# Kernel tuning notes

Hardware: AMD Instinct MI355X
Metric: run time of the kernel (lower is better)

The kernel has to match this reference:

```python
import jax, jax.numpy as jnp
import numpy as np

B, W, KD, NC, D, NN, NH, AD, HOPS = 512, 4, 64, 32, 256, 16, 8, 32, 4
DH = D // NH
DFF = 4 * D
P = B * W + B
ROLE_WRITER, ROLE_QUERY = 0, 1


def setup_inputs() -> dict:
    key = jax.random.key(0)
    ks = iter(jax.random.split(key, 40))
    f = lambda shape, s=0.02: jax.random.normal(next(ks), shape, dtype=jnp.float32) * s
    inp = {
        'query_keys': jax.random.normal(next(ks), (B, KD), dtype=jnp.float32),
        'writer_keys': jax.random.normal(next(ks), (B, W, KD), dtype=jnp.float32),
        'key_proj_w': f((KD, D)), 'key_proj_b': jnp.zeros((D,), jnp.float32),
        'class_embed': f((NC, D)), 'role_embed': f((3, D)), 'start_node_embed': f((NN, D)),
        'input_ln_g': jnp.ones((D,), jnp.float32), 'input_ln_b': jnp.zeros((D,), jnp.float32),
        'ln1_g': jnp.ones((NN, D), jnp.float32), 'ln1_b': jnp.zeros((NN, D), jnp.float32),
        'wqkv': f((NN, D, 3 * D)), 'bqkv': jnp.zeros((NN, 3 * D), jnp.float32),
        'wo': f((NN, D, D)), 'bo': jnp.zeros((NN, D), jnp.float32),
        'ln2_g': jnp.ones((NN, D), jnp.float32), 'ln2_b': jnp.zeros((NN, D), jnp.float32),
        'w_fc1': f((NN, D, DFF)), 'b_fc1': jnp.zeros((NN, DFF), jnp.float32),
        'w_fc2': f((NN, DFF, D)), 'b_fc2': jnp.zeros((NN, D), jnp.float32),
        'delta_w': jnp.zeros((D, D), jnp.float32), 'delta_b': jnp.zeros((D,), jnp.float32),
        'dir_w': f((D, D)), 'dir_b': jnp.zeros((D,), jnp.float32),
        'mag_w': f((D, 1)), 'mag_b': jnp.full((1,), 2.5, jnp.float32),
        'out_w': f((D, NC)), 'out_b': jnp.zeros((NC,), jnp.float32),
        'address_table': jax.random.normal(next(ks), (NN, AD), dtype=jnp.float32),
        'query_start_nodes': jax.random.randint(next(ks), (B,), 0, NN),
        'writer_labels': jax.random.randint(next(ks), (B, W), 0, NC),
        'writer_start_nodes': jax.random.randint(next(ks), (B, W), 0, NN),
    }
    return inp


def _ln(x):
    m = jnp.mean(x, -1, keepdims=True)
    v = jnp.var(x, -1, keepdims=True)
    return (x - m) * jax.lax.rsqrt(v + 1e-5)


def _forward(query_keys, writer_keys, key_proj_w, key_proj_b, class_embed, role_embed,
             start_node_embed, input_ln_g, input_ln_b, ln1_g, ln1_b, wqkv, bqkv, wo, bo,
             ln2_g, ln2_b, w_fc1, b_fc1, w_fc2, b_fc2, delta_w, delta_b, dir_w, dir_b,
             mag_w, mag_b, out_w, out_b, address_table,
             query_start_nodes, writer_labels, writer_start_nodes):
    # ---- encode writers (encode_writers) ----
    fk = writer_keys.reshape(-1, KD)          # [B*W, KD]
    fl = writer_labels.reshape(-1)            # [B*W]
    fs = writer_start_nodes.reshape(-1)       # [B*W]
    learned_w = fk @ key_proj_w + key_proj_b + class_embed[fl] + start_node_embed[fs] + role_embed[ROLE_WRITER]
    sw = jnp.zeros_like(learned_w).at[:, :KD].set(fk)
    sw = sw.at[:, KD:KD + NC].set(jax.nn.one_hot(fl, NC, dtype=learned_w.dtype))
    enc_w = _ln(learned_w) * input_ln_g + input_ln_b + sw
    # ---- encode queries (encode_queries) ----
    learned_q = query_keys @ key_proj_w + key_proj_b + start_node_embed[query_start_nodes] + role_embed[ROLE_QUERY]
    sq = jnp.zeros_like(learned_q).at[:, :KD].set(query_keys)
    enc_q = _ln(learned_q) * input_ln_g + input_ln_b + sq

    h = jnp.concatenate([enc_w, enc_q], axis=0)          # [P, D]
    node = jnp.concatenate([fs, query_start_nodes], 0)   # [P] current compute node per packet

    inv_sqrt_dh = 1.0 / np.sqrt(DH).astype(np.float32)
    for _ in range(HOPS):
        oh = jax.nn.one_hot(node, NN, dtype=h.dtype)      # [P, NN] dispatch weights

        def pnl(x, Wn, bn):
            # per-node linear: gather-compute-scatter via MoE-style dense dispatch
            xe = jnp.einsum('pn,pd->npd', oh, x)          # [NN, P, din]
            ye = jnp.einsum('npd,ndf->npf', xe, Wn)       # [NN, P, dout]
            return jnp.einsum('npf,pn->pf', ye, oh) + oh @ bn

        # ComputeNodeCell: pre-LN attention among packets at the same node
        x = _ln(h) * (oh @ ln1_g) + oh @ ln1_b
        qkv = pnl(x, wqkv, bqkv)                          # [P, 3D]
        q, k, v = jnp.split(qkv, 3, axis=-1)
        q = q.reshape(P, NH, DH); k = k.reshape(P, NH, DH); v = v.reshape(P, NH, DH)
        scores = jnp.einsum('phd,qhd->hpq', q, k) * inv_sqrt_dh   # [NH, P, P]
        same = node[:, None] == node[None, :]
        scores = jnp.where(same[None], scores, -1e9)
        attn = jax.nn.softmax(scores, axis=-1)
        ao = jnp.einsum('hpq,qhd->phd', attn, v).reshape(P, D)
        h = h + pnl(ao, wo, bo)
        # MLP block
        x2 = _ln(h) * (oh @ ln2_g) + oh @ ln2_b
        h = h + pnl(jax.nn.gelu(pnl(x2, w_fc1, b_fc1)), w_fc2, b_fc2)
        # routing heads: pick next node from address table, apply gated delta
        direction = h @ dir_w + dir_b
        node = jnp.argmax(direction[:, :AD] @ address_table.T, axis=-1)
        h = h + (h @ delta_w + delta_b) * jax.nn.sigmoid(h @ mag_w + mag_b)

    return h @ out_w + out_b                              # [P, NC] per-packet logits


def reference(query_keys, writer_keys, key_proj_w, key_proj_b, class_embed, role_embed,
              start_node_embed, input_ln_g, input_ln_b, ln1_g, ln1_b, wqkv, bqkv, wo, bo,
              ln2_g, ln2_b, w_fc1, b_fc1, w_fc2, b_fc2, delta_w, delta_b, dir_w, dir_b,
              mag_w, mag_b, out_w, out_b, address_table,
              query_start_nodes, writer_labels, writer_start_nodes):
    return _forward(query_keys, writer_keys, key_proj_w, key_proj_b, class_embed, role_embed,
                    start_node_embed, input_ln_g, input_ln_b, ln1_g, ln1_b, wqkv, bqkv, wo, bo,
                    ln2_g, ln2_b, w_fc1, b_fc1, w_fc2, b_fc2, delta_w, delta_b, dir_w, dir_b,
                    mag_w, mag_b, out_w, out_b, address_table,
                    query_start_nodes, writer_labels, writer_start_nodes)
```

## Files before the change

### kernel.cpp

```cpp
#include <hip/hip_runtime.h>
#include <math.h>

#define B_    512
#define W_    4
#define KD_   64
#define NC_   32
#define D_    256
#define NN_   16
#define NH_   8
#define AD_   32
#define HOPS_ 4
#define DH_   32
#define DFF_  1024
#define P_    2560
#define BW_   2048
#define MAXT2_ 176

#define INV_SQRT_DH 0.17677669529663687f

__device__ __forceinline__ float block_sum256(float v, float* red) {
#pragma unroll
  for (int off = 32; off > 0; off >>= 1) v += __shfl_xor(v, off, 64);
  int wid = threadIdx.x >> 6;
  if ((threadIdx.x & 63) == 0) red[wid] = v;
  __syncthreads();
  float s = red[0] + red[1] + red[2] + red[3];
  __syncthreads();
  return s;
}

__device__ __forceinline__ float gelu_tanh(float v) {
  float u = 0.7978845608028654f * (v + 0.044715f * v * v * v);
  return 0.5f * v * (1.0f + tanhf(u));
}

__global__ __launch_bounds__(256) void encode_kernel(
    const float* __restrict__ query_keys, const float* __restrict__ writer_keys,
    const float* __restrict__ kpw, const float* __restrict__ kpb,
    const float* __restrict__ ce, const float* __restrict__ re,
    const float* __restrict__ sne, const float* __restrict__ ilg,
    const float* __restrict__ ilb, const int* __restrict__ qsn,
    const int* __restrict__ wl, const int* __restrict__ wsn,
    float* __restrict__ h, int* __restrict__ node) {
  int p = blockIdx.x, t = threadIdx.x;
  __shared__ float fk[KD_];
  __shared__ float red[4];
  const float* key;
  int lab = -1, sn, role;
  if (p < BW_) { key = writer_keys + (size_t)p * KD_; lab = wl[p]; sn = wsn[p]; role = 0; }
  else { int b = p - BW_; key = query_keys + (size_t)b * KD_; sn = qsn[b]; role = 1; }
  if (t < KD_) fk[t] = key[t];
  __syncthreads();

  float acc = kpb[t] + sne[sn * D_ + t] + re[role * D_ + t];
  if (lab >= 0) acc += ce[lab * D_ + t];
#pragma unroll 8
  for (int i = 0; i < KD_; i++) acc += fk[i] * kpw[i * D_ + t];

  float mean = block_sum256(acc, red) * (1.0f / D_);
  float d = acc - mean;
  float var = block_sum256(d * d, red) * (1.0f / D_);
  float xn = d * (1.0f / sqrtf(var + 1e-5f));

  float sw = 0.0f;
  if (t < KD_) sw = fk[t];
  else if (lab >= 0 && t < KD_ + NC_) sw = (t - KD_ == lab) ? 1.0f : 0.0f;

  h[(size_t)p * D_ + t] = xn * ilg[t] + ilb[t] + sw;
  if (t == 0) node[p] = sn;
}

__global__ __launch_bounds__(256) void sort_kernel(const int* __restrict__ node,
                                                   int* __restrict__ order,
                                                   int* __restrict__ invord,
                                                   int* __restrict__ offs,
                                                   int* __restrict__ cnts,
                                                   int* __restrict__ tnode,
                                                   int* __restrict__ tstart,
                                                   int* __restrict__ tend,
                                                   int* __restrict__ ntiles) {
  __shared__ int c[NN_], o[NN_], cur[NN_];
  int t = threadIdx.x;
  if (t < NN_) c[t] = 0;
  __syncthreads();
  for (int p = t; p < P_; p += 256) atomicAdd(&c[node[p]], 1);
  __syncthreads();
  if (t == 0) {
    int s = 0;
    for (int n = 0; n < NN_; n++) { o[n] = s; cur[n] = s; s += c[n]; }
    int idx = 0;
    for (int n = 0; n < NN_; n++) {
      int e = o[n] + c[n];
      for (int m0 = o[n]; m0 < e; m0 += 16) {
        tnode[idx] = n; tstart[idx] = m0; tend[idx] = e; idx++;
      }
    }
    ntiles[0] = idx;
  }
  __syncthreads();
  if (t < NN_) { cnts[t] = c[t]; offs[t] = o[t]; }
  for (int p = t; p < P_; p += 256) {
    int r = atomicAdd(&cur[node[p]], 1);
    order[r] = p;
    invord[p] = r;
  }
}

__global__ __launch_bounds__(256) void ln_affine(const float* __restrict__ h,
                                                 const float* __restrict__ g,
                                                 const float* __restrict__ b,
                                                 const int* __restrict__ node,
                                                 const int* __restrict__ order,
                                                 float* __restrict__ x) {
  int sp = blockIdx.x * 4 + (threadIdx.x >> 6);
  int lane = threadIdx.x & 63;
  int p = order[sp];
  int n = node[p];
  float4 v = *(const float4*)&h[(size_t)p * D_ + lane * 4];
  float s = v.x + v.y + v.z + v.w;
#pragma unroll
  for (int off = 32; off > 0; off >>= 1) s += __shfl_xor(s, off, 64);
  float mean = s * (1.0f / D_);
  float4 d = make_float4(v.x - mean, v.y - mean, v.z - mean, v.w - mean);
  float vr = d.x * d.x + d.y * d.y + d.z * d.z + d.w * d.w;
#pragma unroll
  for (int off = 32; off > 0; off >>= 1) vr += __shfl_xor(vr, off, 64);
  float inv = 1.0f / sqrtf(vr * (1.0f / D_) + 1e-5f);
  float4 gg = *(const float4*)&g[n * D_ + lane * 4];
  float4 bb = *(const float4*)&b[n * D_ + lane * 4];
  float4 o;
  o.x = d.x * inv * gg.x + bb.x;
  o.y = d.y * inv * gg.y + bb.y;
  o.z = d.z * inv * gg.z + bb.z;
  o.w = d.w * inv * gg.w + bb.w;
  *(float4*)&x[(size_t)sp * D_ + lane * 4] = o;
}

template <int DIN, int DOUT, int ACT, int RESID, int PER_NODE, int KSPLIT, int XMODE>
__global__ __launch_bounds__(256) void glin2(const float* __restrict__ x,
                                             const float* __restrict__ W,
                                             const float* __restrict__ bias,
                                             float* __restrict__ out,
                                             float* __restrict__ pbuf,
                                             const float* __restrict__ xaux,
                                             const int* __restrict__ order,
                                             const int* __restrict__ invord,
                                             const int* __restrict__ tnode,
                                             const int* __restrict__ tstart,
                                             const int* __restrict__ tend,
                                             const int* __restrict__ ntiles) {
  constexpr int KLEN = DIN / KSPLIT;

  int gx = gridDim.x;
  int bid = blockIdx.x;
  int ti = (bid & 7) * (gx >> 3) + (bid >> 3);

  int n, s0, rows;
  if (PER_NODE) {
    if (ti >= ntiles[0]) return;
    n = tnode[ti];
    s0 = tstart[ti];
    int e = tend[ti];
    rows = e - s0;
    if (rows > 16) rows = 16;
  } else {
    n = 0;
    s0 = ti * 16;
    rows = 16;
  }
  int jb = blockIdx.y * 256;
  int kz = (KSPLIT > 1) ? blockIdx.z : 0;
  int k0 = kz * KLEN;

  int tid = threadIdx.x;
  int wv = __builtin_amdgcn_readfirstlane((int)(tid >> 6));
  int j4 = (tid & 63) << 2;

  const float* Wp = W + (size_t)n * DIN * DOUT + (size_t)k0 * DOUT + jb + j4;

  const float* xr0;
  const float* xr1;
  const float* xr2;
  const float* xr3;
  const float* ar0 = nullptr;
  const float* ar1 = nullptr;
  const float* ar2 = nullptr;
  const float* ar3 = nullptr;
  {
    int rbase = s0 + (wv << 2);
    xr0 = x + (size_t)(rbase + 0) * DIN + k0;
    xr1 = x + (size_t)(rbase + 1) * DIN + k0;
    xr2 = x + (size_t)(rbase + 2) * DIN + k0;
    xr3 = x + (size_t)(rbase + 3) * DIN + k0;
    if (XMODE == 1) {
      ar0 = xaux + (size_t)invord[rbase + 0] * DIN + k0;
      ar1 = xaux + (size_t)invord[rbase + 1] * DIN + k0;
      ar2 = xaux + (size_t)invord[rbase + 2] * DIN + k0;
      ar3 = xaux + (size_t)invord[rbase + 3] * DIN + k0;
    }
  }

  float4 a0 = make_float4(0.f, 0.f, 0.f, 0.f);
  float4 a1 = a0, a2 = a0, a3 = a0;
  float4 wc0, wc1, wc2, wc3, xc0, xc1, xc2, xc3;

#define LDW_(kk, w0, w1, w2, w3)                              \
  w0 = *(const float4*)(Wp + (size_t)((kk) + 0) * DOUT);      \
  w1 = *(const float4*)(Wp + (size_t)((kk) + 1) * DOUT);      \
  w2 = *(const float4*)(Wp + (size_t)((kk) + 2) * DOUT);      \
  w3 = *(const float4*)(Wp + (size_t)((kk) + 3) * DOUT);

#define LDX1_(kk, ptr, aptr, dst)                             \
  dst = *(const float4*)((ptr) + (kk));                       \
  if (XMODE == 1) {                                           \
    float4 _a = *(const float4*)((aptr) + (kk));              \
    dst.x += _a.x; dst.y += _a.y; dst.z += _a.z; dst.w += _a.w; \
  }

#define LDX_(kk, x0, x1, x2, x3)   \
  LDX1_(kk, xr0, ar0, x0)          \
  LDX1_(kk, xr1, ar1, x1)          \
  LDX1_(kk, xr2, ar2, x2)          \
  LDX1_(kk, xr3, ar3, x3)

  LDW_(0, wc0, wc1, wc2, wc3);
  LDX_(0, xc0, xc1, xc2, xc3);

#pragma unroll 2
  for (int kk = 0; kk < KLEN; kk += 4) {
    float4 wn0, wn1, wn2, wn3, xn0, xn1, xn2, xn3;
    bool more = (kk + 4 < KLEN);
    if (more) {
      LDW_(kk + 4, wn0, wn1, wn2, wn3);
      LDX_(kk + 4, xn0, xn1, xn2, xn3);
    }
#pragma unroll
    for (int t = 0; t < 4; ++t) {
      float4 wt = (t == 0) ? wc0 : (t == 1) ? wc1 : (t == 2) ? wc2 : wc3;
      float f0 = (t == 0) ? xc0.x : (t == 1) ? xc0.y : (t == 2) ? xc0.z : xc0.w;
      float f1 = (t == 0) ? xc1.x : (t == 1) ? xc1.y : (t == 2) ? xc1.z : xc1.w;
      float f2 = (t == 0) ? xc2.x : (t == 1) ? xc2.y : (t == 2) ? xc2.z : xc2.w;
      float f3 = (t == 0) ? xc3.x : (t == 1) ? xc3.y : (t == 2) ? xc3.z : xc3.w;
      a0.x += f0 * wt.x; a0.y += f0 * wt.y; a0.z += f0 * wt.z; a0.w += f0 * wt.w;
      a1.x += f1 * wt.x; a1.y += f1 * wt.y; a1.z += f1 * wt.z; a1.w += f1 * wt.w;
      a2.x += f2 * wt.x; a2.y += f2 * wt.y; a2.z += f2 * wt.z; a2.w += f2 * wt.w;
      a3.x += f3 * wt.x; a3.y += f3 * wt.y; a3.z += f3 * wt.z; a3.w += f3 * wt.w;
    }
    if (more) {
      wc0 = wn0; wc1 = wn1; wc2 = wn2; wc3 = wn3;
      xc0 = xn0; xc1 = xn1; xc2 = xn2; xc3 = xn3;
    }
  }
#undef LDW_
#undef LDX1_
#undef LDX_

  int jcol = jb + j4;
  bool main_part = (KSPLIT == 1) || (kz == 0);
  float4 bv = make_float4(0.f, 0.f, 0.f, 0.f);
  if (main_part) bv = *(const float4*)(bias + (size_t)n * DOUT + jcol);

#pragma unroll
  for (int r = 0; r < 4; ++r) {
    int lr = (wv << 2) + r;
    if (PER_NODE && lr >= rows) continue;
    float4 av = (r == 0) ? a0 : (r == 1) ? a1 : (r == 2) ? a2 : a3;
    if (main_part) {
      float4 v = make_float4(av.x + bv.x, av.y + bv.y, av.z + bv.z, av.w + bv.w);
      if (ACT == 1) {
        v.x = gelu_tanh(v.x); v.y = gelu_tanh(v.y);
        v.z = gelu_tanh(v.z); v.w = gelu_tanh(v.w);
      }
      if (RESID) {
        int pp = PER_NODE ? order[s0 + lr] : (s0 + lr);
        float* op = out + (size_t)pp * DOUT + jcol;
        float4 old = *(const float4*)op;
        *(float4*)op = make_float4(v.x + old.x, v.y + old.y, v.z + old.z, v.w + old.w);
      } else {
        *(float4*)(out + (size_t)(s0 + lr) * DOUT + jcol) = v;
      }
    } else {
      *(float4*)(pbuf + (size_t)(s0 + lr) * DOUT + jcol) = av;
    }
  }
}

#define ATS 36
__global__ __launch_bounds__(256) void attn_kernel(const float* __restrict__ qkv,
                                                   const int* __restrict__ node,
                                                   const int* __restrict__ order,
                                                   const int* __restrict__ offs,
                                                   const int* __restrict__ cnts,
                                                   float* __restrict__ ao) {
  __shared__ float qs[32 * ATS];
  __shared__ float kts[32 * ATS];
  __shared__ float vs[32 * ATS];
  __shared__ float ps[32 * ATS];
  __shared__ int glo[32], ghi[32];

  int t = threadIdx.x;
  int r = t >> 3;
  int j4 = (t & 7) * 4;
  int r0 = blockIdx.x * 32;
  int hd = blockIdx.y;

  if (t < 32) {
    int n = node[order[r0 + t]];
    glo[t] = offs[n];
    ghi[t] = offs[n] + cnts[n];
  }
  __syncthreads();

  {
    const float* qp = &qkv[(size_t)(r0 + r) * 768 + hd * 32 + j4];
    float4 q4 = *(const float4*)qp;
    q4.x *= INV_SQRT_DH; q4.y *= INV_SQRT_DH; q4.z *= INV_SQRT_DH; q4.w *= INV_SQRT_DH;
    *(float4*)&qs[r * ATS + j4] = q4;
  }

  int lo = glo[0];
  int hi = ghi[31];
  int myglo = glo[r], myghi = ghi[r];

  float4 o4 = {0.f, 0.f, 0.f, 0.f};
  float mrow = -1e30f, lrow = 0.f;

  for (int kt = lo; kt < hi; kt += 32) {
    int sj = kt + r;
    float4 k4 = {0.f, 0.f, 0.f, 0.f}, v4 = {0.f, 0.f, 0.f, 0.f};
    if (sj < hi) {
      const float* kp = &qkv[(size_t)sj * 768 + 256 + hd * 32 + j4];
      k4 = *(const float4*)kp;
      v4 = *(const float4*)(kp + 256);
    }
    __syncthreads();
    kts[(j4 + 0) * ATS + r] = k4.x;
    kts[(j4 + 1) * ATS + r] = k4.y;
    kts[(j4 + 2) * ATS + r] = k4.z;
    kts[(j4 + 3) * ATS + r] = k4.w;
    *(float4*)&vs[r * ATS + j4] = v4;
    __syncthreads();

    float s0 = 0.f, s1 = 0.f, s2 = 0.f, s3 = 0.f;
#pragma unroll 8
    for (int d = 0; d < 32; d++) {
      float qv = qs[r * ATS + d];
      float4 kv = *(const float4*)&kts[d * ATS + j4];
      s0 += qv * kv.x; s1 += qv * kv.y; s2 += qv * kv.z; s3 += qv * kv.w;
    }
    int c0 = kt + j4;
    if (c0 + 0 < myglo || c0 + 0 >= myghi) s0 = -1e30f;
    if (c0 + 1 < myglo || c0 + 1 >= myghi) s1 = -1e30f;
    if (c0 + 2 < myglo || c0 + 2 >= myghi) s2 = -1e30f;
    if (c0 + 3 < myglo || c0 + 3 >= myghi) s3 = -1e30f;

    float mx = fmaxf(fmaxf(s0, s1), fmaxf(s2, s3));
#pragma unroll
    for (int off = 4; off > 0; off >>= 1) mx = fmaxf(mx, __shfl_xor(mx, off, 8));
    float mnew = fmaxf(mrow, mx);
    float alpha = __expf(mrow - mnew);
    float p0 = __expf(s0 - mnew), p1 = __expf(s1 - mnew);
    float p2 = __expf(s2 - mnew), p3 = __expf(s3 - mnew);
    float ls = p0 + p1 + p2 + p3;
#pragma unroll
    for (int off = 4; off > 0; off >>= 1) ls += __shfl_xor(ls, off, 8);
    lrow = lrow * alpha + ls;
    mrow = mnew;
    o4.x *= alpha; o4.y *= alpha; o4.z *= alpha; o4.w *= alpha;

    *(float4*)&ps[r * ATS + j4] = make_float4(p0, p1, p2, p3);
#pragma unroll 8
    for (int j = 0; j < 32; j++) {
      float pj = ps[r * ATS + j];
      float4 vv = *(const float4*)&vs[j * ATS + j4];
      o4.x += pj * vv.x; o4.y += pj * vv.y; o4.z += pj * vv.z; o4.w += pj * vv.w;
    }
  }

  float inv = 1.f / lrow;
  o4.x *= inv; o4.y *= inv; o4.z *= inv; o4.w *= inv;
  *(float4*)&ao[(size_t)(r0 + r) * D_ + hd * 32 + j4] = o4;
}

__global__ __launch_bounds__(256) void route_kernel(float* __restrict__ h,
                                                    const float* __restrict__ pbuf,
                                                    const int* __restrict__ invord,
                                                    const float* __restrict__ dir_w,
                                                    const float* __restrict__ dir_b,
                                                    const float* __restrict__ at,
                                                    const float* __restrict__ mag_w,
                                                    const float* __restrict__ mag_b,
                                                    const float* __restrict__ delta,
                                                    int* __restrict__ node) {
  int p = blockIdx.x, t = threadIdx.x;
  __shared__ float hs[D_];
  __shared__ float dpart[8][AD_];
  __shared__ float dirs[AD_];
  __shared__ float scs[NN_];
  __shared__ float red[4];
  float hv = h[(size_t)p * D_ + t] + pbuf[(size_t)invord[p] * D_ + t];
  hs[t] = hv;
  __syncthreads();

  int j = t & 31, seg = t >> 5;
  float part = 0.0f;
#pragma unroll 8
  for (int i = 0; i < 32; i++) {
    int ii = seg * 32 + i;
    part += hs[ii] * dir_w[ii * D_ + j];
  }
  dpart[seg][j] = part;
  __syncthreads();
  if (t < AD_) {
    float s = dir_b[t];
#pragma unroll
    for (int g = 0; g < 8; g++) s += dpart[g][t];
    dirs[t] = s;
  }
  __syncthreads();
  if (t < NN_) {
    float s = 0.0f;
#pragma unroll
    for (int a = 0; a < AD_; a++) s += dirs[a] * at[t * AD_ + a];
    scs[t] = s;
  }
  __syncthreads();
  if (t == 0) {
    float best = scs[0];
    int arg = 0;
    for (int nn = 1; nn < NN_; nn++)
      if (scs[nn] > best) { best = scs[nn]; arg = nn; }
    node[p] = arg;
  }
  float mag = block_sum256(hv * mag_w[t], red) + mag_b[0];
  float sig = 1.0f / (1.0f + __expf(-mag));
  h[(size_t)p * D_ + t] = hv + delta[(size_t)p * D_ + t] * sig;
}

__global__ __launch_bounds__(256) void out_kernel(const float* __restrict__ h,
                                                  const float* __restrict__ ow,
                                                  const float* __restrict__ ob,
                                                  float* __restrict__ out) {
  int p = blockIdx.x, t = threadIdx.x;
  __shared__ float hs[D_];
  __shared__ float part[8][NC_];
  hs[t] = h[(size_t)p * D_ + t];
  __syncthreads();
  int j = t & 31, seg = t >> 5;
  float s = 0.0f;
#pragma unroll 8
  for (int i = 0; i < 32; i++) {
    int ii = seg * 32 + i;
    s += hs[ii] * ow[ii * NC_ + j];
  }
  part[seg][j] = s;
  __syncthreads();
  if (t < NC_) {
    float r = ob[t];
#pragma unroll
    for (int g = 0; g < 8; g++) r += part[g][t];
    out[(size_t)p * NC_ + t] = r;
  }
}

extern "C" void kernel_launch(void* const* d_in, const int* in_sizes, int n_in,
                              void* d_out, int out_size, void* d_ws, size_t ws_size,
                              hipStream_t stream) {
  (void)in_sizes; (void)n_in; (void)out_size; (void)ws_size;
  const float* query_keys       = (const float*)d_in[0];
  const float* writer_keys      = (const float*)d_in[1];
  const float* key_proj_w       = (const float*)d_in[2];
  const float* key_proj_b       = (const float*)d_in[3];
  const float* class_embed      = (const float*)d_in[4];
  const float* role_embed       = (const float*)d_in[5];
  const float* start_node_embed = (const float*)d_in[6];
  const float* input_ln_g       = (const float*)d_in[7];
  const float* input_ln_b       = (const float*)d_in[8];
  const float* ln1_g            = (const float*)d_in[9];
  const float* ln1_b            = (const float*)d_in[10];
  const float* wqkv             = (const float*)d_in[11];
  const float* bqkv             = (const float*)d_in[12];
  const float* wo               = (const float*)d_in[13];
  const float* bo               = (const float*)d_in[14];
  const float* ln2_g            = (const float*)d_in[15];
  const float* ln2_b            = (const float*)d_in[16];
  const float* w_fc1            = (const float*)d_in[17];
  const float* b_fc1            = (const float*)d_in[18];
  const float* w_fc2            = (const float*)d_in[19];
  const float* b_fc2            = (const float*)d_in[20];
  const float* delta_w          = (const float*)d_in[21];
  const float* delta_b          = (const float*)d_in[22];
  const float* dir_w            = (const float*)d_in[23];
  const float* dir_b            = (const float*)d_in[24];
  const float* mag_w            = (const float*)d_in[25];
  const float* mag_b            = (const float*)d_in[26];
  const float* out_w            = (const float*)d_in[27];
  const float* out_b            = (const float*)d_in[28];
  const float* address_table    = (const float*)d_in[29];
  const int* query_start_nodes  = (const int*)d_in[30];
  const int* writer_labels      = (const int*)d_in[31];
  const int* writer_start_nodes = (const int*)d_in[32];

  uintptr_t basep = (uintptr_t)d_ws;
  auto carve = [&](size_t bytes) {
    basep = (basep + 255) & ~(uintptr_t)255;
    void* r = (void*)basep;
    basep += bytes;
    return r;
  };
  float* h    = (float*)carve((size_t)(P_ + 16) * D_ * 4);
  float* x    = (float*)carve((size_t)(P_ + 16) * D_ * 4);
  float* buf1 = (float*)carve((size_t)(P_ + 16) * DFF_ * 4);
  float* ff   = (float*)carve((size_t)(P_ + 16) * DFF_ * 4);
  float* pbuf = (float*)carve((size_t)(P_ + 16) * D_ * 4);
  int* node   = (int*)carve(P_ * 4);
  int* order  = (int*)carve(P_ * 4);
  int* invord = (int*)carve(P_ * 4);
  int* offs   = (int*)carve(NN_ * 4);
  int* cnts   = (int*)carve(NN_ * 4);
  int* tnode  = (int*)carve(MAXT2_ * 4);
  int* tstart = (int*)carve(MAXT2_ * 4);
  int* tend   = (int*)carve(MAXT2_ * 4);
  int* ntiles = (int*)carve(4);

  encode_kernel<<<P_, 256, 0, stream>>>(query_keys, writer_keys, key_proj_w, key_proj_b,
                                        class_embed, role_embed, start_node_embed,
                                        input_ln_g, input_ln_b, query_start_nodes,
                                        writer_labels, writer_start_nodes, h, node);

  for (int hop = 0; hop < HOPS_; ++hop) {
    sort_kernel<<<1, 256, 0, stream>>>(node, order, invord, offs, cnts,
                                       tnode, tstart, tend, ntiles);
    ln_affine<<<P_ / 4, 256, 0, stream>>>(h, ln1_g, ln1_b, node, order, x);
    glin2<256, 768, 0, 0, 1, 1, 0><<<dim3(MAXT2_, 3), 256, 0, stream>>>(
        x, wqkv, bqkv, buf1, nullptr, nullptr, order, invord, tnode, tstart, tend,
        ntiles);
    attn_kernel<<<dim3(P_ / 32, NH_), 256, 0, stream>>>(buf1, node, order, offs,
                                                        cnts, x );
    glin2<256, 256, 0, 1, 1, 1, 0><<<dim3(MAXT2_, 1), 256, 0, stream>>>(
        x, wo, bo, h, nullptr, nullptr, order, invord, tnode, tstart, tend, ntiles);
    ln_affine<<<P_ / 4, 256, 0, stream>>>(h, ln2_g, ln2_b, node, order, x);
    glin2<256, 1024, 1, 0, 1, 1, 0><<<dim3(MAXT2_, 4), 256, 0, stream>>>(
        x, w_fc1, b_fc1, ff, nullptr, nullptr, order, invord, tnode, tstart, tend,
        ntiles);
    glin2<1024, 256, 0, 1, 1, 2, 0><<<dim3(MAXT2_, 1, 2), 256, 0, stream>>>(
        ff, w_fc2, b_fc2, h, pbuf, nullptr, order, invord, tnode, tstart, tend,
        ntiles);
    glin2<256, 256, 0, 0, 0, 1, 1><<<dim3(P_ / 16, 1), 256, 0, stream>>>(
        h, delta_w, delta_b, buf1 , nullptr, pbuf, order, invord,
        tnode, tstart, tend, ntiles);
    route_kernel<<<P_, 256, 0, stream>>>(h, pbuf, invord, dir_w, dir_b, address_table,
                                         mag_w, mag_b, buf1, node);
  }

  out_kernel<<<P_, 256, 0, stream>>>(h, out_w, out_b, (float*)d_out);
}
```

Baseline: 1.079 ms.

## Stage weight tiles in LDS via async global_load_lds with double buffering

Replaces the register-streamed GEMM kernel with one that stages 16-row weight chunks into double-buffered shared memory using direct global-to-LDS loads. Each block now has two waves sharing one weight tile, where before four waves each read weights straight from global memory. The row tile per block is also made configurable, using 8 rows for the smaller projections so they launch more blocks. This should cut redundant global weight traffic and overlap loading with compute, at the cost of a block barrier per chunk and fewer waves per block.

```diff
diff --git a/kernel.cpp b/kernel.cpp
--- a/kernel.cpp
+++ b/kernel.cpp
@@ -136,8 +136,9 @@
   *(float4*)&x[(size_t)sp * D_ + lane * 4] = o;
 }
 
-template <int DIN, int DOUT, int ACT, int RESID, int PER_NODE, int KSPLIT, int XMODE>
-__global__ __launch_bounds__(256) void glin2(const float* __restrict__ x,
+template <int DIN, int DOUT, int RT, int ACT, int RESID, int PER_NODE, int KSPLIT,
+          int XMODE>
+__global__ __launch_bounds__(128) void glin3(const float* __restrict__ x,
                                              const float* __restrict__ W,
                                              const float* __restrict__ bias,
                                              float* __restrict__ out,
@@ -149,7 +150,12 @@
                                              const int* __restrict__ tstart,
                                              const int* __restrict__ tend,
                                              const int* __restrict__ ntiles) {
+  constexpr int KC = 16;
   constexpr int KLEN = DIN / KSPLIT;
+  constexpr int NCH = KLEN / KC;
+  constexpr int RPW = RT / 2;
+
+  __shared__ float ws[2][KC][256];
 
   int gx = gridDim.x;
   int bid = blockIdx.x;
@@ -157,16 +163,18 @@
 
   int n, s0, rows;
   if (PER_NODE) {
-    if (ti >= ntiles[0]) return;
-    n = tnode[ti];
-    s0 = tstart[ti];
-    int e = tend[ti];
+    int tt = (RT == 16) ? ti : (ti >> 1);
+    if (tt >= ntiles[0]) return;
+    n = tnode[tt];
+    s0 = tstart[tt] + ((RT == 8) ? (ti & 1) * 8 : 0);
+    int e = tend[tt];
     rows = e - s0;
-    if (rows > 16) rows = 16;
+    if (rows > RT) rows = RT;
+    if (rows < 0) rows = 0;
   } else {
     n = 0;
-    s0 = ti * 16;
-    rows = 16;
+    s0 = ti * RT;
+    rows = RT;
   }
   int jb = blockIdx.y * 256;
   int kz = (KSPLIT > 1) ? blockIdx.z : 0;
@@ -174,97 +182,91 @@
 
   int tid = threadIdx.x;
   int wv = __builtin_amdgcn_readfirstlane((int)(tid >> 6));
-  int j4 = (tid & 63) << 2;
-
-  const float* Wp = W + (size_t)n * DIN * DOUT + (size_t)k0 * DOUT + jb + j4;
-
-  const float* xr0;
-  const float* xr1;
-  const float* xr2;
-  const float* xr3;
-  const float* ar0 = nullptr;
-  const float* ar1 = nullptr;
-  const float* ar2 = nullptr;
-  const float* ar3 = nullptr;
-  {
-    int rbase = s0 + (wv << 2);
-    xr0 = x + (size_t)(rbase + 0) * DIN + k0;
-    xr1 = x + (size_t)(rbase + 1) * DIN + k0;
-    xr2 = x + (size_t)(rbase + 2) * DIN + k0;
-    xr3 = x + (size_t)(rbase + 3) * DIN + k0;
-    if (XMODE == 1) {
-      ar0 = xaux + (size_t)invord[rbase + 0] * DIN + k0;
-      ar1 = xaux + (size_t)invord[rbase + 1] * DIN + k0;
-      ar2 = xaux + (size_t)invord[rbase + 2] * DIN + k0;
-      ar3 = xaux + (size_t)invord[rbase + 3] * DIN + k0;
-    }
-  }
-
-  float4 a0 = make_float4(0.f, 0.f, 0.f, 0.f);
-  float4 a1 = a0, a2 = a0, a3 = a0;
-  float4 wc0, wc1, wc2, wc3, xc0, xc1, xc2, xc3;
-
-#define LDW_(kk, w0, w1, w2, w3)                              \
-  w0 = *(const float4*)(Wp + (size_t)((kk) + 0) * DOUT);      \
-  w1 = *(const float4*)(Wp + (size_t)((kk) + 1) * DOUT);      \
-  w2 = *(const float4*)(Wp + (size_t)((kk) + 2) * DOUT);      \
-  w3 = *(const float4*)(Wp + (size_t)((kk) + 3) * DOUT);
-
-#define LDX1_(kk, ptr, aptr, dst)                             \
-  dst = *(const float4*)((ptr) + (kk));                       \
-  if (XMODE == 1) {                                           \
-    float4 _a = *(const float4*)((aptr) + (kk));              \
-    dst.x += _a.x; dst.y += _a.y; dst.z += _a.z; dst.w += _a.w; \
-  }
-
-#define LDX_(kk, x0, x1, x2, x3)   \
-  LDX1_(kk, xr0, ar0, x0)          \
-  LDX1_(kk, xr1, ar1, x1)          \
-  LDX1_(kk, xr2, ar2, x2)          \
-  LDX1_(kk, xr3, ar3, x3)
-
-  LDW_(0, wc0, wc1, wc2, wc3);
-  LDX_(0, xc0, xc1, xc2, xc3);
-
-#pragma unroll 2
-  for (int kk = 0; kk < KLEN; kk += 4) {
-    float4 wn0, wn1, wn2, wn3, xn0, xn1, xn2, xn3;
-    bool more = (kk + 4 < KLEN);
-    if (more) {
-      LDW_(kk + 4, wn0, wn1, wn2, wn3);
-      LDX_(kk + 4, xn0, xn1, xn2, xn3);
-    }
-#pragma unroll
-    for (int t = 0; t < 4; ++t) {
-      float4 wt = (t == 0) ? wc0 : (t == 1) ? wc1 : (t == 2) ? wc2 : wc3;
-      float f0 = (t == 0) ? xc0.x : (t == 1) ? xc0.y : (t == 2) ? xc0.z : xc0.w;
-      float f1 = (t == 0) ? xc1.x : (t == 1) ? xc1.y : (t == 2) ? xc1.z : xc1.w;
-      float f2 = (t == 0) ? xc2.x : (t == 1) ? xc2.y : (t == 2) ? xc2.z : xc2.w;
-      float f3 = (t == 0) ? xc3.x : (t == 1) ? xc3.y : (t == 2) ? xc3.z : xc3.w;
-      a0.x += f0 * wt.x; a0.y += f0 * wt.y; a0.z += f0 * wt.z; a0.w += f0 * wt.w;
-      a1.x += f1 * wt.x; a1.y += f1 * wt.y; a1.z += f1 * wt.z; a1.w += f1 * wt.w;
-      a2.x += f2 * wt.x; a2.y += f2 * wt.y; a2.z += f2 * wt.z; a2.w += f2 * wt.w;
-      a3.x += f3 * wt.x; a3.y += f3 * wt.y; a3.z += f3 * wt.z; a3.w += f3 * wt.w;
-    }
-    if (more) {
-      wc0 = wn0; wc1 = wn1; wc2 = wn2; wc3 = wn3;
-      xc0 = xn0; xc1 = xn1; xc2 = xn2; xc3 = xn3;
-    }
-  }
-#undef LDW_
-#undef LDX1_
-#undef LDX_
-
-  int jcol = jb + j4;
+  int lane = tid & 63;
+  int jc = lane << 2;
+
+  const float* Wn = W + (size_t)n * DIN * DOUT + jb;
+
+  auto wstage = [&](int buf, int kc) {
+#pragma unroll
+    for (int i = 0; i < KC / 2; i++) {
+      int kr = wv * (KC / 2) + i;
+      const float* g = Wn + (size_t)(k0 + kc + kr) * DOUT + jc;
+      __builtin_amdgcn_global_load_lds(
+          (const __attribute__((address_space(1))) unsigned int*)g,
+          (__attribute__((address_space(3))) unsigned int*)&ws[buf][kr][0],
+          16, 0, 0);
+    }
+  };
+
+  int rbase = s0 + wv * RPW;
+  const float* xb = x + (size_t)rbase * DIN + k0;
+  const float* ax[RPW];
+  if (XMODE == 1) {
+#pragma unroll
+    for (int r = 0; r < RPW; r++)
+      ax[r] = xaux + (size_t)invord[rbase + r] * DIN + k0;
+  }
+
+  float4 xA[RPW], xB[RPW];
+  auto xfetch = [&](int kk, float4 (&dst)[RPW]) {
+#pragma unroll
+    for (int r = 0; r < RPW; r++) {
+      dst[r] = *(const float4*)(xb + (size_t)r * DIN + kk);
+      if (XMODE == 1) {
+        float4 a = *(const float4*)(ax[r] + kk);
+        dst[r].x += a.x; dst[r].y += a.y; dst[r].z += a.z; dst[r].w += a.w;
+      }
+    }
+  };
+
+  float4 acc[RPW];
+#pragma unroll
+  for (int r = 0; r < RPW; r++) acc[r] = make_float4(0.f, 0.f, 0.f, 0.f);
+
+  auto compute4 = [&](int buf, int kb, float4 (&X)[RPW]) {
+#pragma unroll
+    for (int kq = 0; kq < 4; kq++) {
+      float4 w4 = *(const float4*)&ws[buf][kb + kq][jc];
+#pragma unroll
+      for (int r = 0; r < RPW; r++) {
+        float f = (kq == 0) ? X[r].x : (kq == 1) ? X[r].y : (kq == 2) ? X[r].z : X[r].w;
+        acc[r].x += f * w4.x;
+        acc[r].y += f * w4.y;
+        acc[r].z += f * w4.z;
+        acc[r].w += f * w4.w;
+      }
+    }
+  };
+
+  wstage(0, 0);
+  xfetch(0, xA);
+  __syncthreads();
+
+  for (int c = 0; c < NCH; c++) {
+    int cur = c & 1;
+    if (c + 1 < NCH) wstage(cur ^ 1, (c + 1) * KC);
+    int gk = c * KC;
+#pragma unroll
+    for (int kb = 0; kb < KC; kb += 8) {
+      if (gk + kb + 4 < KLEN) xfetch(gk + kb + 4, xB);
+      compute4(cur, kb, xA);
+      if (gk + kb + 8 < KLEN) xfetch(gk + kb + 8, xA);
+      compute4(cur, kb + 4, xB);
+    }
+    __syncthreads();
+  }
+
+  int jcol = jb + jc;
   bool main_part = (KSPLIT == 1) || (kz == 0);
   float4 bv = make_float4(0.f, 0.f, 0.f, 0.f);
   if (main_part) bv = *(const float4*)(bias + (size_t)n * DOUT + jcol);
 
 #pragma unroll
-  for (int r = 0; r < 4; ++r) {
-    int lr = (wv << 2) + r;
+  for (int r = 0; r < RPW; r++) {
+    int lr = wv * RPW + r;
     if (PER_NODE && lr >= rows) continue;
-    float4 av = (r == 0) ? a0 : (r == 1) ? a1 : (r == 2) ? a2 : a3;
+    float4 av = acc[r];
     if (main_part) {
       float4 v = make_float4(av.x + bv.x, av.y + bv.y, av.z + bv.z, av.w + bv.w);
       if (ACT == 1) {
@@ -532,21 +534,21 @@
     sort_kernel<<<1, 256, 0, stream>>>(node, order, invord, offs, cnts,
                                        tnode, tstart, tend, ntiles);
     ln_affine<<<P_ / 4, 256, 0, stream>>>(h, ln1_g, ln1_b, node, order, x);
-    glin2<256, 768, 0, 0, 1, 1, 0><<<dim3(MAXT2_, 3), 256, 0, stream>>>(
+    glin3<256, 768, 16, 0, 0, 1, 1, 0><<<dim3(MAXT2_, 3), 128, 0, stream>>>(
         x, wqkv, bqkv, buf1, nullptr, nullptr, order, invord, tnode, tstart, tend,
         ntiles);
     attn_kernel<<<dim3(P_ / 32, NH_), 256, 0, stream>>>(buf1, node, order, offs,
                                                         cnts, x );
-    glin2<256, 256, 0, 1, 1, 1, 0><<<dim3(MAXT2_, 1), 256, 0, stream>>>(
+    glin3<256, 256, 8, 0, 1, 1, 1, 0><<<dim3(MAXT2_ * 2, 1), 128, 0, stream>>>(
         x, wo, bo, h, nullptr, nullptr, order, invord, tnode, tstart, tend, ntiles);
     ln_affine<<<P_ / 4, 256, 0, stream>>>(h, ln2_g, ln2_b, node, order, x);
-    glin2<256, 1024, 1, 0, 1, 1, 0><<<dim3(MAXT2_, 4), 256, 0, stream>>>(
+    glin3<256, 1024, 16, 1, 0, 1, 1, 0><<<dim3(MAXT2_, 4), 128, 0, stream>>>(
         x, w_fc1, b_fc1, ff, nullptr, nullptr, order, invord, tnode, tstart, tend,
         ntiles);
-    glin2<1024, 256, 0, 1, 1, 2, 0><<<dim3(MAXT2_, 1, 2), 256, 0, stream>>>(
+    glin3<1024, 256, 16, 0, 1, 1, 2, 0><<<dim3(MAXT2_, 1, 2), 128, 0, stream>>>(
         ff, w_fc2, b_fc2, h, pbuf, nullptr, order, invord, tnode, tstart, tend,
         ntiles);
-    glin2<256, 256, 0, 0, 0, 1, 1><<<dim3(P_ / 16, 1), 256, 0, stream>>>(
+    glin3<256, 256, 8, 0, 0, 0, 1, 1><<<dim3(P_ / 8, 1), 128, 0, stream>>>(
         h, delta_w, delta_b, buf1 , nullptr, pbuf, order, invord,
         tnode, tstart, tend, ntiles);
     route_kernel<<<P_, 256, 0, stream>>>(h, pbuf, invord, dir_w, dir_b, address_table,
```

Result: slower. 1.643 ms (+52.3%).
